# Performance work log

Hardware: AMD Instinct MI355X
Metric: run time of the kernel (lower is better)

## Reference

```python
import jax, jax.numpy as jnp
import numpy as np

S, B, D, W = 2048, 4, 1024, 256  # seq_len, batch, d_model, local_window_size


def create_local_mask(seq_len, w):
    # Faithful to source: tril(w-1) then tril(-(w-1)) -> keeps j <= i-(w-1)
    m = jnp.ones((seq_len, seq_len), dtype=bool)
    m = jnp.tril(m, w - 1)
    m = jnp.tril(m, -(w - 1))
    return m


def setup_inputs() -> dict:
    key = jax.random.key(0)
    ks = jax.random.split(key, 12)
    w = lambda k: jax.random.normal(k, (D, D), dtype=jnp.float32) * 0.02
    return {
        "query": jax.random.normal(ks[0], (S, B, D), dtype=jnp.float32),
        "key_in": jax.random.normal(ks[1], (S, B, D), dtype=jnp.float32),
        "value": jax.random.normal(ks[2], (S, B, D), dtype=jnp.float32),
        "Wq": w(ks[3]), "bq": jnp.zeros((D,), jnp.float32),
        "Wk": w(ks[4]), "bk": jnp.zeros((D,), jnp.float32),
        "Wv": w(ks[5]), "bv": jnp.zeros((D,), jnp.float32),
        "pos_bias": jax.random.normal(ks[6], (S, S), dtype=jnp.float32) * 0.02,
        "Wo": w(ks[7]), "bo": jnp.zeros((D,), jnp.float32),
        "mask": jnp.ones((S, S, 1), dtype=bool),
    }


def reference(query, key_in, value, Wq, bq, Wk, bk, Wv, bv, pos_bias, Wo, bo, mask):
    # Linear projections (torch Linear: x @ W.T + b)
    q = jnp.einsum('sbd,ed->sbe', query, Wq) + bq
    k = jnp.einsum('sbd,ed->sbe', key_in, Wk) + bk
    v = jnp.einsum('sbd,ed->sbe', value, Wv) + bv

    local_mask = create_local_mask(S, W)
    pb = (pos_bias * local_mask.astype(pos_bias.dtype))[:, :, None]  # [S,S,1]
    pb = jnp.where(mask, pb, -jnp.inf)

    max_key = jnp.max(k, axis=0, keepdims=True)          # [1,B,D]
    max_pb = jnp.max(pb, axis=1, keepdims=True)          # [S,1,1]
    exp_key = jnp.exp(k - max_key)                       # [S,B,D]
    exp_pb = jnp.exp(pb - max_pb)                        # [S,S,B] after broadcast

    num = jnp.einsum('ijb,jbd->ibd', exp_pb, exp_key * v)
    den = jnp.einsum('ijb,jbd->ibd', exp_pb, exp_key)
    y = jax.nn.sigmoid(q) * num / den
    return jnp.einsum('sbd,ed->sbe', y, Wo) + bo
```

## Files before the change

kernel.cpp:

```cpp
#include <hip/hip_runtime.h>
#include <hip/hip_bf16.h>
#include <cstdint>


typedef short short8 __attribute__((ext_vector_type(8)));
typedef float f32x4 __attribute__((ext_vector_type(4)));

#define S_LEN 2048
#define NBD 4096
#define SBD 8388608
#define DD 1048576
#define SS 4194304

__device__ __forceinline__ unsigned short f2bf(float f) {
  union { float f; unsigned int u; } x; x.f = f;
  unsigned int u = x.u;
  unsigned int r = u + 0x7fffu + ((u >> 16) & 1u);
  return (unsigned short)(r >> 16);
}
__device__ __forceinline__ float bf2f(unsigned short b) {
  union { unsigned int u; float f; } x; x.u = ((unsigned int)b) << 16;
  return x.f;
}

__global__ void k_cvt3(const float* __restrict__ a, const float* __restrict__ b,
                       const float* __restrict__ c, unsigned short* __restrict__ oa,
                       unsigned short* __restrict__ ob, unsigned short* __restrict__ oc) {
  int i = (blockIdx.x * blockDim.x + threadIdx.x) * 4;
  float4 fa = *(const float4*)(a + i);
  float4 fb = *(const float4*)(b + i);
  float4 fc = *(const float4*)(c + i);
  ushort4 ua, ub, uc;
  ua.x = f2bf(fa.x); ua.y = f2bf(fa.y); ua.z = f2bf(fa.z); ua.w = f2bf(fa.w);
  ub.x = f2bf(fb.x); ub.y = f2bf(fb.y); ub.z = f2bf(fb.z); ub.w = f2bf(fb.w);
  uc.x = f2bf(fc.x); uc.y = f2bf(fc.y); uc.z = f2bf(fc.z); uc.w = f2bf(fc.w);
  *(ushort4*)(oa + i) = ua;
  *(ushort4*)(ob + i) = ub;
  *(ushort4*)(oc + i) = uc;
}

__global__ void k_cvt4w(const float* __restrict__ wq, const float* __restrict__ wk,
                        const float* __restrict__ wv, const float* __restrict__ wo,
                        unsigned short* __restrict__ wcat, unsigned short* __restrict__ wob) {
  int i = (blockIdx.x * blockDim.x + threadIdx.x) * 4;
  float4 fq = *(const float4*)(wq + i);
  float4 fk = *(const float4*)(wk + i);
  float4 fv = *(const float4*)(wv + i);
  float4 fo = *(const float4*)(wo + i);
  ushort4 u;
  u.x = f2bf(fq.x); u.y = f2bf(fq.y); u.z = f2bf(fq.z); u.w = f2bf(fq.w);
  *(ushort4*)(wcat + i) = u;
  u.x = f2bf(fk.x); u.y = f2bf(fk.y); u.z = f2bf(fk.z); u.w = f2bf(fk.w);
  *(ushort4*)(wcat + DD + i) = u;
  u.x = f2bf(fv.x); u.y = f2bf(fv.y); u.z = f2bf(fv.z); u.w = f2bf(fv.w);
  *(ushort4*)(wcat + 2 * DD + i) = u;
  u.x = f2bf(fo.x); u.y = f2bf(fo.y); u.z = f2bf(fo.z); u.w = f2bf(fo.w);
  *(ushort4*)(wob + i) = u;
}

__global__ void k_build_c(const float* __restrict__ pb, unsigned short* __restrict__ C) {
  int idx = blockIdx.x * blockDim.x + threadIdx.x;
  int i = idx >> 11;
  int j = idx & 2047;
  float v = (i >= j + 255) ? expm1f(pb[idx]) : 0.0f;
  C[idx] = f2bf(v);
}

__global__ __launch_bounds__(256) void k_eu_transpose(
    const unsigned short* __restrict__ kbf, const unsigned short* __restrict__ vbf,
    unsigned short* __restrict__ Mt, float* __restrict__ totals) {
  __shared__ unsigned short Lu[64][65];
  __shared__ unsigned short Le[64][65];
  const int n0 = blockIdx.x * 64;
  const int j0 = blockIdx.y * 64;
  const int t = threadIdx.x;
  const int c = t & 63;
  const int jq = t >> 6;
  float ptu = 0.f, pte = 0.f;
#pragma unroll 4
  for (int s = 0; s < 16; ++s) {
    int jj = jq + s * 4;
    size_t g = (size_t)(j0 + jj) * NBD + n0 + c;
    float kv = bf2f(kbf[g]);
    float vv = bf2f(vbf[g]);
    float e = __expf(kv);
    float u = e * vv;
    Le[jj][c] = f2bf(e);
    Lu[jj][c] = f2bf(u);
    pte += e; ptu += u;
  }
  atomicAdd(&totals[n0 + c], ptu);
  atomicAdd(&totals[NBD + n0 + c], pte);
  __syncthreads();
  const int jj2 = t & 63;
  const int nq = t >> 6;
#pragma unroll 4
  for (int s = 0; s < 16; ++s) {
    int nn = nq + s * 4;
    int ru = 2 * n0 + 32 * (nn >> 4) + (nn & 15);
    Mt[(size_t)ru * S_LEN + j0 + jj2] = Lu[jj2][nn];
    Mt[(size_t)(ru + 16) * S_LEN + j0 + jj2] = Le[jj2][nn];
  }
}

__global__ __launch_bounds__(256) void k_gemm_qkv(
    const unsigned short* __restrict__ A0, const unsigned short* __restrict__ A1,
    const unsigned short* __restrict__ A2, const unsigned short* __restrict__ Wcat,
    const float* __restrict__ b0, const float* __restrict__ b1, const float* __restrict__ b2,
    unsigned short* __restrict__ o0, unsigned short* __restrict__ o1,
    unsigned short* __restrict__ o2) {
  __shared__ __align__(16) unsigned short lab[128 * 32];
  __shared__ __align__(16) unsigned short lbb[128 * 32];
  const int tid = threadIdx.x;
  const int wave = tid >> 6, lane = tid & 63;
  const int w = blockIdx.x;
  const int xcd = w & 7, slot = w >> 3;
  const int mb = xcd * 8 + slot / 24;
  const int nb = slot % 24;
  const int m0 = mb * 128, n0 = nb * 128;
  const int grp = nb >> 3;
  const unsigned short* A = grp == 0 ? A0 : (grp == 1 ? A1 : A2);
  const float* bias = grp == 0 ? b0 : (grp == 1 ? b1 : b2);
  unsigned short* out = grp == 0 ? o0 : (grp == 1 ? o1 : o2);
  const int l15 = lane & 15, lh = lane >> 4;
  const int wr = (wave >> 1) * 64, wc = (wave & 1) * 64;

  f32x4 acc[4][4];
#pragma unroll
  for (int i = 0; i < 4; ++i)
#pragma unroll
    for (int j = 0; j < 4; ++j)
      acc[i][j] = (f32x4){0.f, 0.f, 0.f, 0.f};

  const int srow = lane >> 2;
  const int scol = (lane & 3) * 8;

  for (int kt = 0; kt < 32; ++kt) {
    const int k0 = kt * 32;
    if (kt) __syncthreads();
#pragma unroll
    for (int cdx = 0; cdx < 2; ++cdx) {
      const int seg = wave * 2 + cdx;
      const int row = seg * 16 + srow;
      __builtin_amdgcn_global_load_lds(
          (const __attribute__((address_space(1))) unsigned int*)(A + (size_t)(m0 + row) * 1024 + k0 + scol),
          (__attribute__((address_space(3))) unsigned int*)&lab[seg * 512], 16, 0, 0);
      __builtin_amdgcn_global_load_lds(
          (const __attribute__((address_space(1))) unsigned int*)(Wcat + (size_t)(n0 + row) * 1024 + k0 + scol),
          (__attribute__((address_space(3))) unsigned int*)&lbb[seg * 512], 16, 0, 0);
    }
    __syncthreads();
    short8 af[4], bfr[4];
#pragma unroll
    for (int f = 0; f < 4; ++f)
      af[f] = *(const short8*)&lab[(wr + f * 16 + l15) * 32 + lh * 8];
#pragma unroll
    for (int f = 0; f < 4; ++f)
      bfr[f] = *(const short8*)&lbb[(wc + f * 16 + l15) * 32 + lh * 8];
#pragma unroll
    for (int i = 0; i < 4; ++i)
#pragma unroll
      for (int j = 0; j < 4; ++j)
        acc[i][j] = __builtin_amdgcn_mfma_f32_16x16x32_bf16(af[i], bfr[j], acc[i][j], 0, 0, 0);
  }

#pragma unroll
  for (int i = 0; i < 4; ++i)
#pragma unroll
    for (int j = 0; j < 4; ++j)
#pragma unroll
      for (int r = 0; r < 4; ++r) {
        const int row = m0 + wr + i * 16 + lh * 4 + r;
        const int col = (n0 + wc + j * 16 + l15) & 1023;
        float v = acc[i][j][r] + bias[col];
        if (grp == 0) v = 1.0f / (1.0f + __expf(-v));
        out[(size_t)row * 1024 + col] = f2bf(v);
      }
}

__global__ __launch_bounds__(256) void k_gemm_tri(
    const unsigned short* __restrict__ A, const unsigned short* __restrict__ Bt,
    const unsigned short* __restrict__ sigq, const float* __restrict__ totals,
    unsigned short* __restrict__ Y) {
  __shared__ __align__(16) unsigned short lab[128 * 32];
  __shared__ __align__(16) unsigned short lbb[128 * 32];
  const int tid = threadIdx.x;
  const int wave = tid >> 6, lane = tid & 63;
  const int w = blockIdx.x;
  const int mb = 15 - (w >> 6);
  const int nb = w & 63;
  const int m0 = mb * 128, n0 = nb * 128;
  const int l15 = lane & 15, lh = lane >> 4;
  const int wr = (wave >> 1) * 64, wc = (wave & 1) * 64;

  f32x4 acc[4][4];
#pragma unroll
  for (int i = 0; i < 4; ++i)
#pragma unroll
    for (int j = 0; j < 4; ++j)
      acc[i][j] = (f32x4){0.f, 0.f, 0.f, 0.f};

  const int nk = mb > 0 ? 4 * mb - 3 : 0;
  const int srow = lane >> 2;
  const int scol = (lane & 3) * 8;

  for (int kt = 0; kt < nk; ++kt) {
    const int k0 = kt * 32;
    if (kt) __syncthreads();
#pragma unroll
    for (int cdx = 0; cdx < 2; ++cdx) {
      const int seg = wave * 2 + cdx;
      const int row = seg * 16 + srow;
      __builtin_amdgcn_global_load_lds(
          (const __attribute__((address_space(1))) unsigned int*)(A + (size_t)(m0 + row) * S_LEN + k0 + scol),
          (__attribute__((address_space(3))) unsigned int*)&lab[seg * 512], 16, 0, 0);
      __builtin_amdgcn_global_load_lds(
          (const __attribute__((address_space(1))) unsigned int*)(Bt + (size_t)(n0 + row) * S_LEN + k0 + scol),
          (__attribute__((address_space(3))) unsigned int*)&lbb[seg * 512], 16, 0, 0);
    }
    __syncthreads();
    short8 af[4], bfr[4];
#pragma unroll
    for (int f = 0; f < 4; ++f)
      af[f] = *(const short8*)&lab[(wr + f * 16 + l15) * 32 + lh * 8];
#pragma unroll
    for (int f = 0; f < 4; ++f)
      bfr[f] = *(const short8*)&lbb[(wc + f * 16 + l15) * 32 + lh * 8];
#pragma unroll
    for (int i = 0; i < 4; ++i)
#pragma unroll
      for (int j = 0; j < 4; ++j)
        acc[i][j] = __builtin_amdgcn_mfma_f32_16x16x32_bf16(af[i], bfr[j], acc[i][j], 0, 0, 0);
  }

#pragma unroll
  for (int i = 0; i < 4; ++i)
#pragma unroll
    for (int p = 0; p < 2; ++p) {
      const int n = 64 * nb + (2 * (wave & 1) + p) * 16 + l15;
      const float tu = totals[n];
      const float te = totals[NBD + n];
#pragma unroll
      for (int r = 0; r < 4; ++r) {
        const int row = m0 + wr + i * 16 + lh * 4 + r;
        const size_t idx = (size_t)row * NBD + n;
        const float num = tu + acc[i][2 * p][r];
        const float den = te + acc[i][2 * p + 1][r];
        Y[idx] = f2bf(bf2f(sigq[idx]) * num / den);
      }
    }
}

__global__ __launch_bounds__(256) void k_gemm_out64(
    const unsigned short* __restrict__ A, const unsigned short* __restrict__ Bt,
    const float* __restrict__ bias, float* __restrict__ out) {
  __shared__ __align__(16) unsigned short laa[64 * 32];
  __shared__ __align__(16) unsigned short lbb[128 * 32];
  const int tid = threadIdx.x;
  const int wave = tid >> 6, lane = tid & 63;
  const int w = blockIdx.x;
  const int xcd = w & 7, slot = w >> 3;
  const int mb = xcd * 16 + (slot >> 3);
  const int nb = slot & 7;
  const int m0 = mb * 64, n0 = nb * 128;
  const int l15 = lane & 15, lh = lane >> 4;
  const int wr = (wave >> 1) * 32, wc = (wave & 1) * 64;

  f32x4 acc[2][4];
#pragma unroll
  for (int i = 0; i < 2; ++i)
#pragma unroll
    for (int j = 0; j < 4; ++j)
      acc[i][j] = (f32x4){0.f, 0.f, 0.f, 0.f};

  const int srow = lane >> 2;
  const int scol = (lane & 3) * 8;

  for (int kt = 0; kt < 32; ++kt) {
    const int k0 = kt * 32;
    if (kt) __syncthreads();
    {
      const int row = wave * 16 + srow;
      __builtin_amdgcn_global_load_lds(
          (const __attribute__((address_space(1))) unsigned int*)(A + (size_t)(m0 + row) * 1024 + k0 + scol),
          (__attribute__((address_space(3))) unsigned int*)&laa[wave * 512], 16, 0, 0);
    }
#pragma unroll
    for (int cdx = 0; cdx < 2; ++cdx) {
      const int seg = wave * 2 + cdx;
      const int row = seg * 16 + srow;
      __builtin_amdgcn_global_load_lds(
          (const __attribute__((address_space(1))) unsigned int*)(Bt + (size_t)(n0 + row) * 1024 + k0 + scol),
          (__attribute__((address_space(3))) unsigned int*)&lbb[seg * 512], 16, 0, 0);
    }
    __syncthreads();
    short8 af[2], bfr[4];
#pragma unroll
    for (int f = 0; f < 2; ++f)
      af[f] = *(const short8*)&laa[(wr + f * 16 + l15) * 32 + lh * 8];
#pragma unroll
    for (int f = 0; f < 4; ++f)
      bfr[f] = *(const short8*)&lbb[(wc + f * 16 + l15) * 32 + lh * 8];
#pragma unroll
    for (int i = 0; i < 2; ++i)
#pragma unroll
      for (int j = 0; j < 4; ++j)
        acc[i][j] = __builtin_amdgcn_mfma_f32_16x16x32_bf16(af[i], bfr[j], acc[i][j], 0, 0, 0);
  }

#pragma unroll
  for (int i = 0; i < 2; ++i)
#pragma unroll
    for (int j = 0; j < 4; ++j)
#pragma unroll
      for (int r = 0; r < 4; ++r) {
        const int row = m0 + wr + i * 16 + lh * 4 + r;
        const int col = n0 + wc + j * 16 + l15;
        out[(size_t)row * 1024 + col] = acc[i][j][r] + bias[col];
      }
}

extern "C" void kernel_launch(void* const* d_in, const int* in_sizes, int n_in,
                              void* d_out, int out_size, void* d_ws, size_t ws_size,
                              hipStream_t stream) {
  const float* query   = (const float*)d_in[0];
  const float* key_in  = (const float*)d_in[1];
  const float* value   = (const float*)d_in[2];
  const float* Wq      = (const float*)d_in[3];
  const float* bq      = (const float*)d_in[4];
  const float* Wk      = (const float*)d_in[5];
  const float* bk      = (const float*)d_in[6];
  const float* Wv      = (const float*)d_in[7];
  const float* bv      = (const float*)d_in[8];
  const float* pos_bias= (const float*)d_in[9];
  const float* Wo      = (const float*)d_in[10];
  const float* bo      = (const float*)d_in[11];
  float* out = (float*)d_out;

  char* wp = (char*)d_ws;
  auto alloc = [&](size_t bytes) -> char* {
    char* p = wp;
    wp += (bytes + 255) & ~(size_t)255;
    return p;
  };
  unsigned short* Xq   = (unsigned short*)alloc((size_t)SBD * 2);
  unsigned short* Xk   = (unsigned short*)alloc((size_t)SBD * 2);
  unsigned short* Xv   = (unsigned short*)alloc((size_t)SBD * 2);
  unsigned short* Wcat = (unsigned short*)alloc((size_t)3 * DD * 2);
  unsigned short* Wob  = (unsigned short*)alloc((size_t)DD * 2);
  unsigned short* Cb   = (unsigned short*)alloc((size_t)SS * 2);
  unsigned short* sigq = (unsigned short*)alloc((size_t)SBD * 2);
  unsigned short* kbf  = (unsigned short*)alloc((size_t)SBD * 2);
  unsigned short* vbf  = (unsigned short*)alloc((size_t)SBD * 2);
  unsigned short* Mt   = (unsigned short*)alloc((size_t)8192 * S_LEN * 2);
  float*          tot  = (float*)alloc((size_t)8192 * 4);
  unsigned short* Yb   = (unsigned short*)alloc((size_t)SBD * 2);

  k_cvt3<<<SBD / 4 / 256, 256, 0, stream>>>(query, key_in, value, Xq, Xk, Xv);
  k_cvt4w<<<DD / 4 / 256, 256, 0, stream>>>(Wq, Wk, Wv, Wo, Wcat, Wob);

  k_build_c<<<SS / 256, 256, 0, stream>>>(pos_bias, Cb);

  k_gemm_qkv<<<1536, 256, 0, stream>>>(Xq, Xk, Xv, Wcat, bq, bk, bv, sigq, kbf, vbf);

  hipMemsetAsync(tot, 0, 8192 * sizeof(float), stream);
  dim3 ge(NBD / 64, S_LEN / 64);
  k_eu_transpose<<<ge, 256, 0, stream>>>(kbf, vbf, Mt, tot);

  k_gemm_tri<<<1024, 256, 0, stream>>>(Cb, Mt, sigq, tot, Yb);

  k_gemm_out64<<<1024, 256, 0, stream>>>(Yb, Wob, bo, out);
}
```

Baseline: 209.0 us.

## Unify GEMMs into triple-buffered 128x256 kernel with swizzled LDS and prefetch

Replaces the three separate single-buffered 128x128 (and 64x128) bf16 MFMA GEMM kernels with one templated 512-thread kernel. It uses 128x256 tiles, a 64-wide K step, a three-stage LDS ring filled by global_load_lds, and XOR-swizzled LDS addressing. It interleaves register double-buffered fragment reads with MFMAs, using explicit vmcnt waits and setprio. The aim is to hide global latency, reduce barrier count and LDS bank conflicts, and raise data reuse per tile. In exchange it uses more LDS and registers per block and gives fewer blocks for the smaller GEMMs.

```diff
diff --git a/kernel.cpp b/kernel.cpp
--- a/kernel.cpp
+++ b/kernel.cpp
@@ -11,6 +11,11 @@
 #define SBD 8388608
 #define DD 1048576
 #define SS 4194304
+
+#define ASZ 8192
+#define BUFSZ 24576
+#define AS1 __attribute__((address_space(1)))
+#define AS3 __attribute__((address_space(3)))
 
 __device__ __forceinline__ unsigned short f2bf(float f) {
   union { float f; unsigned int u; } x; x.f = f;
@@ -103,27 +108,80 @@
   }
 }
 
-__global__ __launch_bounds__(256) void k_gemm_qkv(
+
+#define SBAR() do { __builtin_amdgcn_sched_barrier(0); __builtin_amdgcn_s_barrier(); \
+                    __builtin_amdgcn_sched_barrier(0); } while (0)
+#define VM(n)  do { asm volatile("s_waitcnt vmcnt(" #n ")" ::: "memory"); \
+                    __builtin_amdgcn_sched_barrier(0); } while (0)
+#define LGK0() do { asm volatile("s_waitcnt lgkmcnt(0)" ::: "memory"); \
+                    __builtin_amdgcn_sched_barrier(0); } while (0)
+
+#define STAGE(tile, bidx) do {                                                            \
+    const int k0s_ = (tile) * 64;                                                         \
+    _Pragma("unroll") for (int q_ = 0; q_ < 2; ++q_) {                                    \
+      const int g_ = wave * 2 + q_;                                                       \
+      __builtin_amdgcn_global_load_lds(                                                   \
+          (const AS1 unsigned int*)(Ag + (size_t)(m0 + g_ * 8 + lr) * LDA + k0s_ + lc),   \
+          (AS3 unsigned int*)&lds[(bidx) * BUFSZ + g_ * 512], 16, 0, 0);                  \
+    }                                                                                     \
+    _Pragma("unroll") for (int q_ = 0; q_ < 4; ++q_) {                                    \
+      const int g_ = wave * 4 + q_;                                                       \
+      __builtin_amdgcn_global_load_lds(                                                   \
+          (const AS1 unsigned int*)(Bg + (size_t)(n0 + g_ * 8 + lr) * LDB + k0s_ + lc),   \
+          (AS3 unsigned int*)&lds[(bidx) * BUFSZ + ASZ + g_ * 512], 16, 0, 0);            \
+    }                                                                                     \
+  } while (0)
+
+#define READF(RA, RB, bidx, ks) do {                                                      \
+    const int kof_ = (ks) * 32 + lh8;                                                     \
+    _Pragma("unroll") for (int f_ = 0; f_ < 4; ++f_) {                                    \
+      const int row_ = wr + f_ * 16 + l15;                                                \
+      RA[f_] = *(const short8*)&lds[(bidx) * BUFSZ + row_ * 64 + (kof_ ^ swz)];           \
+    }                                                                                     \
+    _Pragma("unroll") for (int f_ = 0; f_ < 4; ++f_) {                                    \
+      const int row_ = wc + f_ * 16 + l15;                                                \
+      RB[f_] = *(const short8*)&lds[(bidx) * BUFSZ + ASZ + row_ * 64 + (kof_ ^ swz)];     \
+    }                                                                                     \
+  } while (0)
+
+#define MFMA16(RA, RB) do {                                                               \
+    __builtin_amdgcn_s_setprio(1);                                                        \
+    _Pragma("unroll") for (int i_ = 0; i_ < 4; ++i_)                                      \
+    _Pragma("unroll") for (int j_ = 0; j_ < 4; ++j_)                                      \
+      acc[i_][j_] = __builtin_amdgcn_mfma_f32_16x16x32_bf16(RA[i_], RB[j_],               \
+                                                            acc[i_][j_], 0, 0, 0);       \
+    __builtin_amdgcn_s_setprio(0);                                                        \
+  } while (0)
+
+template <int MODE>
+__global__ __launch_bounds__(512, 2) void k_gemm8(
     const unsigned short* __restrict__ A0, const unsigned short* __restrict__ A1,
-    const unsigned short* __restrict__ A2, const unsigned short* __restrict__ Wcat,
-    const float* __restrict__ b0, const float* __restrict__ b1, const float* __restrict__ b2,
-    unsigned short* __restrict__ o0, unsigned short* __restrict__ o1,
-    unsigned short* __restrict__ o2) {
-  __shared__ __align__(16) unsigned short lab[128 * 32];
-  __shared__ __align__(16) unsigned short lbb[128 * 32];
+    const unsigned short* __restrict__ A2, const unsigned short* __restrict__ Bg,
+    const float* __restrict__ x0, const float* __restrict__ x1, const float* __restrict__ x2,
+    const unsigned short* __restrict__ sq,
+    void* __restrict__ out0, void* __restrict__ out1, void* __restrict__ out2) {
+  __shared__ unsigned short lds[3 * BUFSZ];
+
   const int tid = threadIdx.x;
   const int wave = tid >> 6, lane = tid & 63;
+  const int l15 = lane & 15, lh = lane >> 4;
+  const int lh8 = lh * 8;
+  const int swz = (l15 & 7) * 8;
+  const int lr = lane >> 3;
+  const int lc = ((lane & 7) ^ lr) * 8;
+  const int wr = (wave >> 2) * 64, wc = (wave & 3) * 64;
+
   const int w = blockIdx.x;
-  const int xcd = w & 7, slot = w >> 3;
-  const int mb = xcd * 8 + slot / 24;
-  const int nb = slot % 24;
-  const int m0 = mb * 128, n0 = nb * 128;
-  const int grp = nb >> 3;
-  const unsigned short* A = grp == 0 ? A0 : (grp == 1 ? A1 : A2);
-  const float* bias = grp == 0 ? b0 : (grp == 1 ? b1 : b2);
-  unsigned short* out = grp == 0 ? o0 : (grp == 1 ? o1 : o2);
-  const int l15 = lane & 15, lh = lane >> 4;
-  const int wr = (wave >> 1) * 64, wc = (wave & 1) * 64;
+  int mb, nb;
+  if (MODE == 0) { const int xcd = w & 7, slot = w >> 3; mb = xcd * 8 + slot / 12; nb = slot % 12; }
+  else if (MODE == 1) { mb = 15 - (w >> 5); nb = w & 31; }
+  else { const int xcd = w & 7, slot = w >> 3; mb = xcd * 8 + (slot >> 2); nb = slot & 3; }
+  const int m0 = mb * 128, n0 = nb * 256;
+  const int LDA = (MODE == 1) ? 2048 : 1024;
+  const int LDB = (MODE == 1) ? 2048 : 1024;
+  const int NT = (MODE == 1) ? (mb > 0 ? 2 * mb - 1 : 0) : 16;
+  const int grp = (MODE == 0) ? (nb >> 2) : 0;
+  const unsigned short* Ag = (MODE == 0) ? (grp == 0 ? A0 : (grp == 1 ? A1 : A2)) : A0;
 
   f32x4 acc[4][4];
 #pragma unroll
@@ -132,192 +190,80 @@
     for (int j = 0; j < 4; ++j)
       acc[i][j] = (f32x4){0.f, 0.f, 0.f, 0.f};
 
-  const int srow = lane >> 2;
-  const int scol = (lane & 3) * 8;
-
-  for (int kt = 0; kt < 32; ++kt) {
-    const int k0 = kt * 32;
-    if (kt) __syncthreads();
-#pragma unroll
-    for (int cdx = 0; cdx < 2; ++cdx) {
-      const int seg = wave * 2 + cdx;
-      const int row = seg * 16 + srow;
-      __builtin_amdgcn_global_load_lds(
-          (const __attribute__((address_space(1))) unsigned int*)(A + (size_t)(m0 + row) * 1024 + k0 + scol),
-          (__attribute__((address_space(3))) unsigned int*)&lab[seg * 512], 16, 0, 0);
-      __builtin_amdgcn_global_load_lds(
-          (const __attribute__((address_space(1))) unsigned int*)(Wcat + (size_t)(n0 + row) * 1024 + k0 + scol),
-          (__attribute__((address_space(3))) unsigned int*)&lbb[seg * 512], 16, 0, 0);
-    }
-    __syncthreads();
-    short8 af[4], bfr[4];
-#pragma unroll
-    for (int f = 0; f < 4; ++f)
-      af[f] = *(const short8*)&lab[(wr + f * 16 + l15) * 32 + lh * 8];
-#pragma unroll
-    for (int f = 0; f < 4; ++f)
-      bfr[f] = *(const short8*)&lbb[(wc + f * 16 + l15) * 32 + lh * 8];
-#pragma unroll
-    for (int i = 0; i < 4; ++i)
-#pragma unroll
-      for (int j = 0; j < 4; ++j)
-        acc[i][j] = __builtin_amdgcn_mfma_f32_16x16x32_bf16(af[i], bfr[j], acc[i][j], 0, 0, 0);
-  }
-
-#pragma unroll
-  for (int i = 0; i < 4; ++i)
-#pragma unroll
-    for (int j = 0; j < 4; ++j)
-#pragma unroll
-      for (int r = 0; r < 4; ++r) {
-        const int row = m0 + wr + i * 16 + lh * 4 + r;
-        const int col = (n0 + wc + j * 16 + l15) & 1023;
-        float v = acc[i][j][r] + bias[col];
-        if (grp == 0) v = 1.0f / (1.0f + __expf(-v));
-        out[(size_t)row * 1024 + col] = f2bf(v);
-      }
-}
-
-__global__ __launch_bounds__(256) void k_gemm_tri(
-    const unsigned short* __restrict__ A, const unsigned short* __restrict__ Bt,
-    const unsigned short* __restrict__ sigq, const float* __restrict__ totals,
-    unsigned short* __restrict__ Y) {
-  __shared__ __align__(16) unsigned short lab[128 * 32];
-  __shared__ __align__(16) unsigned short lbb[128 * 32];
-  const int tid = threadIdx.x;
-  const int wave = tid >> 6, lane = tid & 63;
-  const int w = blockIdx.x;
-  const int mb = 15 - (w >> 6);
-  const int nb = w & 63;
-  const int m0 = mb * 128, n0 = nb * 128;
-  const int l15 = lane & 15, lh = lane >> 4;
-  const int wr = (wave >> 1) * 64, wc = (wave & 1) * 64;
-
-  f32x4 acc[4][4];
-#pragma unroll
-  for (int i = 0; i < 4; ++i)
-#pragma unroll
-    for (int j = 0; j < 4; ++j)
-      acc[i][j] = (f32x4){0.f, 0.f, 0.f, 0.f};
-
-  const int nk = mb > 0 ? 4 * mb - 3 : 0;
-  const int srow = lane >> 2;
-  const int scol = (lane & 3) * 8;
-
-  for (int kt = 0; kt < nk; ++kt) {
-    const int k0 = kt * 32;
-    if (kt) __syncthreads();
-#pragma unroll
-    for (int cdx = 0; cdx < 2; ++cdx) {
-      const int seg = wave * 2 + cdx;
-      const int row = seg * 16 + srow;
-      __builtin_amdgcn_global_load_lds(
-          (const __attribute__((address_space(1))) unsigned int*)(A + (size_t)(m0 + row) * S_LEN + k0 + scol),
-          (__attribute__((address_space(3))) unsigned int*)&lab[seg * 512], 16, 0, 0);
-      __builtin_amdgcn_global_load_lds(
-          (const __attribute__((address_space(1))) unsigned int*)(Bt + (size_t)(n0 + row) * S_LEN + k0 + scol),
-          (__attribute__((address_space(3))) unsigned int*)&lbb[seg * 512], 16, 0, 0);
-    }
-    __syncthreads();
-    short8 af[4], bfr[4];
-#pragma unroll
-    for (int f = 0; f < 4; ++f)
-      af[f] = *(const short8*)&lab[(wr + f * 16 + l15) * 32 + lh * 8];
-#pragma unroll
-    for (int f = 0; f < 4; ++f)
-      bfr[f] = *(const short8*)&lbb[(wc + f * 16 + l15) * 32 + lh * 8];
-#pragma unroll
-    for (int i = 0; i < 4; ++i)
-#pragma unroll
-      for (int j = 0; j < 4; ++j)
-        acc[i][j] = __builtin_amdgcn_mfma_f32_16x16x32_bf16(af[i], bfr[j], acc[i][j], 0, 0, 0);
-  }
-
-#pragma unroll
-  for (int i = 0; i < 4; ++i)
-#pragma unroll
-    for (int p = 0; p < 2; ++p) {
-      const int n = 64 * nb + (2 * (wave & 1) + p) * 16 + l15;
-      const float tu = totals[n];
-      const float te = totals[NBD + n];
-#pragma unroll
-      for (int r = 0; r < 4; ++r) {
-        const int row = m0 + wr + i * 16 + lh * 4 + r;
-        const size_t idx = (size_t)row * NBD + n;
-        const float num = tu + acc[i][2 * p][r];
-        const float den = te + acc[i][2 * p + 1][r];
-        Y[idx] = f2bf(bf2f(sigq[idx]) * num / den);
+  short8 ra0[4], rb0[4], ra1[4], rb1[4];
+
+  if (NT > 0) {
+    STAGE(0, 0);
+    if (NT > 1) STAGE(1, 1);
+    if (NT > 2) STAGE(2, 2);
+    if (NT > 2) VM(12); else if (NT > 1) VM(6); else VM(0);
+    SBAR();
+    READF(ra0, rb0, 0, 0);
+    int cb = 0;
+    for (int t = 0; t < NT; ++t) {
+      READF(ra1, rb1, cb, 1);
+      MFMA16(ra0, rb0);
+      if (t < NT - 1) {
+        LGK0();
+        if (t + 2 <= NT - 1) VM(6); else VM(0);
+        SBAR();
+        int nbuf = cb + 1; if (nbuf == 3) nbuf = 0;
+        READF(ra0, rb0, nbuf, 0);
+        if (t + 3 <= NT - 1) STAGE(t + 3, cb);
+        cb = nbuf;
+        MFMA16(ra1, rb1);
+      } else {
+        MFMA16(ra1, rb1);
       }
     }
-}
-
-__global__ __launch_bounds__(256) void k_gemm_out64(
-    const unsigned short* __restrict__ A, const unsigned short* __restrict__ Bt,
-    const float* __restrict__ bias, float* __restrict__ out) {
-  __shared__ __align__(16) unsigned short laa[64 * 32];
-  __shared__ __align__(16) unsigned short lbb[128 * 32];
-  const int tid = threadIdx.x;
-  const int wave = tid >> 6, lane = tid & 63;
-  const int w = blockIdx.x;
-  const int xcd = w & 7, slot = w >> 3;
-  const int mb = xcd * 16 + (slot >> 3);
-  const int nb = slot & 7;
-  const int m0 = mb * 64, n0 = nb * 128;
-  const int l15 = lane & 15, lh = lane >> 4;
-  const int wr = (wave >> 1) * 32, wc = (wave & 1) * 64;
-
-  f32x4 acc[2][4];
-#pragma unroll
-  for (int i = 0; i < 2; ++i)
-#pragma unroll
-    for (int j = 0; j < 4; ++j)
-      acc[i][j] = (f32x4){0.f, 0.f, 0.f, 0.f};
-
-  const int srow = lane >> 2;
-  const int scol = (lane & 3) * 8;
-
-  for (int kt = 0; kt < 32; ++kt) {
-    const int k0 = kt * 32;
-    if (kt) __syncthreads();
-    {
-      const int row = wave * 16 + srow;
-      __builtin_amdgcn_global_load_lds(
-          (const __attribute__((address_space(1))) unsigned int*)(A + (size_t)(m0 + row) * 1024 + k0 + scol),
-          (__attribute__((address_space(3))) unsigned int*)&laa[wave * 512], 16, 0, 0);
-    }
-#pragma unroll
-    for (int cdx = 0; cdx < 2; ++cdx) {
-      const int seg = wave * 2 + cdx;
-      const int row = seg * 16 + srow;
-      __builtin_amdgcn_global_load_lds(
-          (const __attribute__((address_space(1))) unsigned int*)(Bt + (size_t)(n0 + row) * 1024 + k0 + scol),
-          (__attribute__((address_space(3))) unsigned int*)&lbb[seg * 512], 16, 0, 0);
-    }
-    __syncthreads();
-    short8 af[2], bfr[4];
-#pragma unroll
-    for (int f = 0; f < 2; ++f)
-      af[f] = *(const short8*)&laa[(wr + f * 16 + l15) * 32 + lh * 8];
-#pragma unroll
-    for (int f = 0; f < 4; ++f)
-      bfr[f] = *(const short8*)&lbb[(wc + f * 16 + l15) * 32 + lh * 8];
-#pragma unroll
-    for (int i = 0; i < 2; ++i)
+  }
+
+  if (MODE == 0) {
+    const float* bias = grp == 0 ? x0 : (grp == 1 ? x1 : x2);
+    unsigned short* outp = (unsigned short*)(grp == 0 ? out0 : (grp == 1 ? out1 : out2));
+#pragma unroll
+    for (int i = 0; i < 4; ++i)
 #pragma unroll
       for (int j = 0; j < 4; ++j)
-        acc[i][j] = __builtin_amdgcn_mfma_f32_16x16x32_bf16(af[i], bfr[j], acc[i][j], 0, 0, 0);
+#pragma unroll
+        for (int r = 0; r < 4; ++r) {
+          const int row = m0 + wr + i * 16 + lh * 4 + r;
+          const int col = (n0 + wc + j * 16 + l15) & 1023;
+          float v = acc[i][j][r] + bias[col];
+          if (grp == 0) v = 1.0f / (1.0f + __expf(-v));
+          outp[(size_t)row * 1024 + col] = f2bf(v);
+        }
+  } else if (MODE == 1) {
+    unsigned short* Y = (unsigned short*)out0;
+#pragma unroll
+    for (int i = 0; i < 4; ++i)
+#pragma unroll
+      for (int p = 0; p < 2; ++p) {
+        const int n = ((n0 + wc) >> 1) + 16 * p + l15;
+        const float tu = x0[n];
+        const float te = x0[NBD + n];
+#pragma unroll
+        for (int r = 0; r < 4; ++r) {
+          const int row = m0 + wr + i * 16 + lh * 4 + r;
+          const size_t idx = (size_t)row * NBD + n;
+          const float num = tu + acc[i][2 * p][r];
+          const float den = te + acc[i][2 * p + 1][r];
+          Y[idx] = f2bf(bf2f(sq[idx]) * num / den);
+        }
+      }
+  } else {
+    float* outp = (float*)out0;
+#pragma unroll
+    for (int i = 0; i < 4; ++i)
+#pragma unroll
+      for (int j = 0; j < 4; ++j)
+#pragma unroll
+        for (int r = 0; r < 4; ++r) {
+          const int row = m0 + wr + i * 16 + lh * 4 + r;
+          const int col = n0 + wc + j * 16 + l15;
+          outp[(size_t)row * 1024 + col] = acc[i][j][r] + x0[col];
+        }
   }
-
-#pragma unroll
-  for (int i = 0; i < 2; ++i)
-#pragma unroll
-    for (int j = 0; j < 4; ++j)
-#pragma unroll
-      for (int r = 0; r < 4; ++r) {
-        const int row = m0 + wr + i * 16 + lh * 4 + r;
-        const int col = n0 + wc + j * 16 + l15;
-        out[(size_t)row * 1024 + col] = acc[i][j][r] + bias[col];
-      }
 }
 
 extern "C" void kernel_launch(void* const* d_in, const int* in_sizes, int n_in,
@@ -361,13 +307,16 @@
 
   k_build_c<<<SS / 256, 256, 0, stream>>>(pos_bias, Cb);
 
-  k_gemm_qkv<<<1536, 256, 0, stream>>>(Xq, Xk, Xv, Wcat, bq, bk, bv, sigq, kbf, vbf);
+  k_gemm8<0><<<768, 512, 0, stream>>>(Xq, Xk, Xv, Wcat, bq, bk, bv, nullptr,
+                                      sigq, kbf, vbf);
 
   hipMemsetAsync(tot, 0, 8192 * sizeof(float), stream);
   dim3 ge(NBD / 64, S_LEN / 64);
   k_eu_transpose<<<ge, 256, 0, stream>>>(kbf, vbf, Mt, tot);
 
-  k_gemm_tri<<<1024, 256, 0, stream>>>(Cb, Mt, sigq, tot, Yb);
-
-  k_gemm_out64<<<1024, 256, 0, stream>>>(Yb, Wob, bo, out);
-}
+  k_gemm8<1><<<512, 512, 0, stream>>>(Cb, nullptr, nullptr, Mt, tot, nullptr, nullptr,
+                                      sigq, Yb, nullptr, nullptr);
+
+  k_gemm8<2><<<256, 512, 0, stream>>>(Yb, nullptr, nullptr, Wob, bo, nullptr, nullptr,
+                                      nullptr, out, nullptr, nullptr);
+}
```

New measurement: 179.6 us. -14.1%, faster.
